# Performance work log

Hardware: AMD Instinct MI355X
Metric: run time of the kernel (lower is better)

## Reference

```python
import jax, jax.numpy as jnp
import numpy as np
from functools import partial

DN = jax.lax.conv_dimension_numbers((1, 1, 3, 3), (1, 1, 3, 3), ('NCHW', 'OIHW', 'NCHW'))


def setup_inputs() -> dict:
    key = jax.random.key(0)
    ks = jax.random.split(key, 5)
    x = jax.random.normal(ks[0], (16, 1, 512, 512), dtype=jnp.float32)
    k = jax.random.normal(ks[1], (1, 1, 3, 3), dtype=jnp.float32)
    w1 = jax.random.normal(ks[2], (10, 1), dtype=jnp.float32) * 0.5
    b1 = jax.random.normal(ks[3], (10,), dtype=jnp.float32) * 0.1
    w2 = jax.random.normal(ks[4], (1, 10), dtype=jnp.float32) * 0.5
    return {"x": x, "k": k, "w1": w1, "b1": b1, "w2": w2, "steps": 16}


def _step(x, k, w1, b1, w2):
    # 3x3 stencil, 1 channel, SAME padding, no bias
    out = jax.lax.conv_general_dilated(x, k, (1, 1), 'SAME', dimension_numbers=DN)
    # gaussian activation
    out = jnp.exp(-(out - 1.0) ** 2)
    # pointwise MLP: 1 -> 10 (ReLU) -> 1 (Sigmoid)
    h = jax.nn.relu(jnp.einsum('bchw,oc->bohw', out, w1) + b1[None, :, None, None])
    out = jax.nn.sigmoid(jnp.einsum('bchw,oc->bohw', h, w2))
    # residual update
    return x + (out - 0.5)


def reference(x, k, w1, b1, w2, steps):
    def body(x, _):
        x_new = _step(x, k, w1, b1, w2)
        return x_new, x_new

    _, seq = jax.lax.scan(body, x, None, length=steps)
    # prepend initial state: [steps+1, B, 1, H, W]
    return jnp.concatenate([x[None], seq], axis=0)
```

## Files before the change

### kernel.cpp

```cpp
#include <hip/hip_runtime.h>


#define NCA_H 512
#define NCA_W 512
#define NCA_HW (NCA_H * NCA_W)

__global__ __launch_bounds__(256) void nca_step(const float* __restrict__ src,
                                                float* __restrict__ dst,
                                                const float* __restrict__ kc,
                                                const float* __restrict__ w1,
                                                const float* __restrict__ b1,
                                                const float* __restrict__ w2) {
    __shared__ float sk[9], sw1[10], sb1[10], sw2[10];
    {
        int t = threadIdx.x;
        if (t < 9)  sk[t]  = kc[t];
        if (t < 10) { sw1[t] = w1[t]; sb1[t] = b1[t]; sw2[t] = w2[t]; }
    }
    __syncthreads();

    int idx = blockIdx.x * blockDim.x + threadIdx.x;
    int wq = idx & 127;
    int h  = (idx >> 7) & 511;
    int b  = idx >> 16;
    int w0 = wq << 2;

    const float* base = src + (size_t)b * NCA_HW;

    float rowv[3][6];
#pragma unroll
    for (int r = 0; r < 3; ++r) {
        int hh = h + r - 1;
        if (hh < 0 || hh >= NCA_H) {
#pragma unroll
            for (int c = 0; c < 6; ++c) rowv[r][c] = 0.f;
        } else {
            const float* rp = base + hh * NCA_W + w0;
            float4 c4 = *(const float4*)rp;
            rowv[r][1] = c4.x; rowv[r][2] = c4.y; rowv[r][3] = c4.z; rowv[r][4] = c4.w;
            rowv[r][0] = (w0 > 0) ? rp[-1] : 0.f;
            rowv[r][5] = (w0 + 4 < NCA_W) ? rp[4] : 0.f;
        }
    }

    float4 res;
    float* resp = (float*)&res;
#pragma unroll
    for (int j = 0; j < 4; ++j) {
        float s = 0.f;
#pragma unroll
        for (int r = 0; r < 3; ++r) {
            s = fmaf(sk[r * 3 + 0], rowv[r][j],     s);
            s = fmaf(sk[r * 3 + 1], rowv[r][j + 1], s);
            s = fmaf(sk[r * 3 + 2], rowv[r][j + 2], s);
        }
        float d = s - 1.0f;
        float g = __expf(-d * d);
        float acc = 0.f;
#pragma unroll
        for (int o = 0; o < 10; ++o) {
            float hm = fmaxf(fmaf(sw1[o], g, sb1[o]), 0.f);
            acc = fmaf(sw2[o], hm, acc);
        }
        float sig = __fdividef(1.0f, 1.0f + __expf(-acc));
        resp[j] = rowv[1][j + 1] + (sig - 0.5f);
    }

    *(float4*)(dst + (size_t)b * NCA_HW + h * NCA_W + w0) = res;
}

extern "C" void kernel_launch(void* const* d_in, const int* in_sizes, int n_in,
                              void* d_out, int out_size, void* d_ws, size_t ws_size,
                              hipStream_t stream) {
    const float* x  = (const float*)d_in[0];
    const float* k  = (const float*)d_in[1];
    const float* w1 = (const float*)d_in[2];
    const float* b1 = (const float*)d_in[3];
    const float* w2 = (const float*)d_in[4];
    float* out = (float*)d_out;

    const int slice = in_sizes[0];
    const int steps = out_size / slice - 1;

    hipMemcpyAsync(out, x, (size_t)slice * sizeof(float),
                   hipMemcpyDeviceToDevice, stream);

    const int threads = 256;
    const int blocks  = slice / 4 / threads;
    for (int t = 0; t < steps; ++t) {
        nca_step<<<blocks, threads, 0, stream>>>(out + (size_t)t * slice,
                                                 out + (size_t)(t + 1) * slice,
                                                 k, w1, b1, w2);
    }
}
```

Measured before the change: 450.8 us.

## Fuse eight time steps per launch using shared-memory tiles with halo

Each launch now keeps an 80x80 tile (a 64x64 interior plus an 8-cell halo) in double-buffered shared memory and advances it up to 8 steps, writing each step's interior to the trajectory. This removes the per-step global read of the previous state and cuts the launch count from 16 to 2. In exchange it recomputes the halo region (about 56% extra work per tile), adds a block barrier per step, and leaves only 240 of 256 threads active.

```diff
diff --git a/kernel.cpp b/kernel.cpp
--- a/kernel.cpp
+++ b/kernel.cpp
@@ -4,69 +4,113 @@
 #define NCA_H 512
 #define NCA_W 512
 #define NCA_HW (NCA_H * NCA_W)
+#define TX 80
+#define HALO 8
+#define NG 20
+#define NACT 240
 
-__global__ __launch_bounds__(256) void nca_step(const float* __restrict__ src,
-                                                float* __restrict__ dst,
-                                                const float* __restrict__ kc,
-                                                const float* __restrict__ w1,
-                                                const float* __restrict__ b1,
-                                                const float* __restrict__ w2) {
-    __shared__ float sk[9], sw1[10], sb1[10], sw2[10];
-    {
-        int t = threadIdx.x;
-        if (t < 9)  sk[t]  = kc[t];
-        if (t < 10) { sw1[t] = w1[t]; sb1[t] = b1[t]; sw2[t] = w2[t]; }
+__global__ __launch_bounds__(256) void nca_fused(float* __restrict__ traj,
+                                                 size_t slice,
+                                                 int nsteps,
+                                                 const float* __restrict__ kc,
+                                                 const float* __restrict__ w1v,
+                                                 const float* __restrict__ b1v,
+                                                 const float* __restrict__ w2v) {
+    __shared__ float buf[2][TX * TX];
+
+    float kk[9];
+#pragma unroll
+    for (int i = 0; i < 9; ++i) kk[i] = kc[i];
+    float rw1[10], rb1[10], rw2[10];
+#pragma unroll
+    for (int o = 0; o < 10; ++o) { rw1[o] = w1v[o]; rb1[o] = b1v[o]; rw2[o] = w2v[o]; }
+
+    const int bi = blockIdx.x;
+    const int b  = bi >> 6;
+    const int ty = (bi >> 3) & 7;
+    const int tx = bi & 7;
+    const int gh0 = ty * 64 - HALO;
+    const int gw0 = tx * 64 - HALO;
+
+    const float* sp = traj + (size_t)b * NCA_HW;
+    for (int i = threadIdx.x; i < (TX * TX / 4); i += 256) {
+        int row = i / NG;
+        int c4  = i - row * NG;
+        int gh  = gh0 + row;
+        int gw  = gw0 + 4 * c4;
+        float4 v = make_float4(0.f, 0.f, 0.f, 0.f);
+        if (((unsigned)gh < NCA_H) && ((unsigned)gw < NCA_W))
+            v = *(const float4*)(sp + (size_t)gh * NCA_W + gw);
+        *(float4*)&buf[0][row * TX + 4 * c4] = v;
+    }
+    if (threadIdx.x < 2 * NG) {
+        int row = (threadIdx.x < NG) ? 0 : (TX - 1);
+        int c4  = threadIdx.x % NG;
+        *(float4*)&buf[1][row * TX + 4 * c4] = make_float4(0.f, 0.f, 0.f, 0.f);
     }
     __syncthreads();
 
-    int idx = blockIdx.x * blockDim.x + threadIdx.x;
-    int wq = idx & 127;
-    int h  = (idx >> 7) & 511;
-    int b  = idx >> 16;
-    int w0 = wq << 2;
+    const int tid = threadIdx.x;
+    const bool active = tid < NACT;
+    const int g  = tid % NG;
+    const int rb = tid / NG;
+    const int w0 = g * 4;
+    const int r0 = (rb < 6) ? (1 + 7 * rb) : (43 + 6 * (rb - 6));
+    const int r1 = r0 + ((rb < 6) ? 7 : 6);
+    const bool colStore = active && (w0 >= HALO) && (w0 < TX - HALO);
+    const bool colIn = ((unsigned)(gw0 + w0) < NCA_W);
+    const int wl = (w0 > 0) ? (w0 - 1) : 0;
+    const int wr = (w0 + 4 < TX) ? (w0 + 4) : (TX - 1);
 
-    const float* base = src + (size_t)b * NCA_HW;
-
-    float rowv[3][6];
+    int cur = 0;
+    for (int s = 1; s <= nsteps; ++s) {
+        const float* cb = buf[cur];
+        float* nb = buf[cur ^ 1];
+        float* gout = traj + (size_t)s * slice + (size_t)b * NCA_HW;
+        if (active) {
+            for (int r = r0; r < r1; ++r) {
+                const bool ok = colIn && ((unsigned)(gh0 + r) < NCA_H);
+                float rv[3][6];
 #pragma unroll
-    for (int r = 0; r < 3; ++r) {
-        int hh = h + r - 1;
-        if (hh < 0 || hh >= NCA_H) {
+                for (int rr = 0; rr < 3; ++rr) {
+                    const float* rp = cb + (r - 1 + rr) * TX;
+                    float4 c4v = *(const float4*)(rp + w0);
+                    rv[rr][0] = rp[wl];
+                    rv[rr][1] = c4v.x; rv[rr][2] = c4v.y;
+                    rv[rr][3] = c4v.z; rv[rr][4] = c4v.w;
+                    rv[rr][5] = rp[wr];
+                }
+                float4 res;
+                float* resp = (float*)&res;
 #pragma unroll
-            for (int c = 0; c < 6; ++c) rowv[r][c] = 0.f;
-        } else {
-            const float* rp = base + hh * NCA_W + w0;
-            float4 c4 = *(const float4*)rp;
-            rowv[r][1] = c4.x; rowv[r][2] = c4.y; rowv[r][3] = c4.z; rowv[r][4] = c4.w;
-            rowv[r][0] = (w0 > 0) ? rp[-1] : 0.f;
-            rowv[r][5] = (w0 + 4 < NCA_W) ? rp[4] : 0.f;
+                for (int j = 0; j < 4; ++j) {
+                    float sacc = 0.f;
+#pragma unroll
+                    for (int rr = 0; rr < 3; ++rr) {
+                        sacc = fmaf(kk[rr * 3 + 0], rv[rr][j],     sacc);
+                        sacc = fmaf(kk[rr * 3 + 1], rv[rr][j + 1], sacc);
+                        sacc = fmaf(kk[rr * 3 + 2], rv[rr][j + 2], sacc);
+                    }
+                    float d = sacc - 1.0f;
+                    float gg = __expf(-d * d);
+                    float acc = 0.f;
+#pragma unroll
+                    for (int o = 0; o < 10; ++o) {
+                        float hm = fmaxf(fmaf(rw1[o], gg, rb1[o]), 0.f);
+                        acc = fmaf(rw2[o], hm, acc);
+                    }
+                    float sig = __fdividef(1.0f, 1.0f + __expf(-acc));
+                    float val = rv[1][j + 1] + (sig - 0.5f);
+                    resp[j] = ok ? val : 0.f;
+                }
+                *(float4*)&nb[r * TX + w0] = res;
+                if (colStore && r >= HALO && r < TX - HALO)
+                    *(float4*)(gout + (size_t)(gh0 + r) * NCA_W + (gw0 + w0)) = res;
+            }
         }
+        __syncthreads();
+        cur ^= 1;
     }
-
-    float4 res;
-    float* resp = (float*)&res;
-#pragma unroll
-    for (int j = 0; j < 4; ++j) {
-        float s = 0.f;
-#pragma unroll
-        for (int r = 0; r < 3; ++r) {
-            s = fmaf(sk[r * 3 + 0], rowv[r][j],     s);
-            s = fmaf(sk[r * 3 + 1], rowv[r][j + 1], s);
-            s = fmaf(sk[r * 3 + 2], rowv[r][j + 2], s);
-        }
-        float d = s - 1.0f;
-        float g = __expf(-d * d);
-        float acc = 0.f;
-#pragma unroll
-        for (int o = 0; o < 10; ++o) {
-            float hm = fmaxf(fmaf(sw1[o], g, sb1[o]), 0.f);
-            acc = fmaf(sw2[o], hm, acc);
-        }
-        float sig = __fdividef(1.0f, 1.0f + __expf(-acc));
-        resp[j] = rowv[1][j + 1] + (sig - 0.5f);
-    }
-
-    *(float4*)(dst + (size_t)b * NCA_HW + h * NCA_W + w0) = res;
 }
 
 extern "C" void kernel_launch(void* const* d_in, const int* in_sizes, int n_in,
@@ -79,17 +123,17 @@
     const float* w2 = (const float*)d_in[4];
     float* out = (float*)d_out;
 
-    const int slice = in_sizes[0];
-    const int steps = out_size / slice - 1;
+    const size_t slice = (size_t)in_sizes[0];
+    const int steps = out_size / (int)slice - 1;
+    const int B = (int)(slice / NCA_HW);
 
-    hipMemcpyAsync(out, x, (size_t)slice * sizeof(float),
-                   hipMemcpyDeviceToDevice, stream);
+    hipMemcpyAsync(out, x, slice * sizeof(float), hipMemcpyDeviceToDevice, stream);
 
-    const int threads = 256;
-    const int blocks  = slice / 4 / threads;
-    for (int t = 0; t < steps; ++t) {
-        nca_step<<<blocks, threads, 0, stream>>>(out + (size_t)t * slice,
-                                                 out + (size_t)(t + 1) * slice,
-                                                 k, w1, b1, w2);
+    const int blocks = B * 64;
+    for (int base = 0; base < steps; base += HALO) {
+        int ns = steps - base;
+        if (ns > HALO) ns = HALO;
+        nca_fused<<<blocks, 256, 0, stream>>>(out + (size_t)base * slice, slice, ns,
+                                              k, w1, b1, w2);
     }
 }
```

New measurement: 480.0 us. 6.5% more time.
